# Kernel optimization log

Hardware: AMD Instinct MI355X
Metric: run time of the kernel (lower is better)

Reference implementation:

```python
import jax, jax.numpy as jnp
import numpy as np

B, T, E = 4, 2048, 1024
H, D = 16, 64


def setup_inputs() -> dict:
    key = jax.random.key(0)
    ks = jax.random.split(key, 7)
    scale = 1.0 / np.sqrt(E)
    return {
        "query": jax.random.normal(ks[0], (B, T, E), jnp.float32),
        "key_": jax.random.normal(ks[1], (B, T, E), jnp.float32),
        "value": jax.random.normal(ks[2], (B, T, E), jnp.float32),
        # nn.Linear weights have shape (out_features, in_features); y = x @ W.T
        "Wq": jax.random.normal(ks[3], (H * D, E), jnp.float32) * scale,
        "Wk": jax.random.normal(ks[4], (H * D, E), jnp.float32) * scale,
        "Wv": jax.random.normal(ks[5], (H * D, E), jnp.float32) * scale,
        "Wo": jax.random.normal(ks[6], (E, H * D), jnp.float32) * scale,
    }


def reference(query, key_, value, Wq, Wk, Wv, Wo):
    # eval mode: dropout is identity
    Bq, Tq, _ = query.shape
    Q = (query @ Wq.T).reshape(Bq, Tq, H, D).transpose(0, 2, 1, 3)   # [B,H,T,D]
    K = (key_ @ Wk.T).reshape(Bq, -1, H, D).transpose(0, 2, 1, 3)    # [B,H,S,D]
    V = (value @ Wv.T).reshape(Bq, -1, H, D).transpose(0, 2, 1, 3)   # [B,H,S,D]
    scores = jnp.einsum("bhtd,bhsd->bhts", Q, K) / jnp.sqrt(jnp.float32(D))
    attn_prob = jax.nn.softmax(scores, axis=-1)                      # [B,H,T,S]
    attn_vec = jnp.einsum("bhts,bhsd->bhtd", attn_prob, V)           # [B,H,T,D]
    x = attn_vec.transpose(0, 2, 1, 3).reshape(Bq, Tq, H * D) @ Wo.T # [B,T,E]
    # need_weights=True, average_attn_weights=True -> mean over heads
    return x, attn_prob.mean(axis=1)
```

## Files before the change

kernel.cpp:

```cpp
#include <hip/hip_runtime.h>
#include <math.h>

#define HH 16
#define DD 64
#define TS 2048
#define EE 1024
#define BB 4
#define MS 12.0f

typedef __attribute__((ext_vector_type(8))) __bf16 bf16x8;
typedef __attribute__((ext_vector_type(2))) __bf16 bf16x2;
typedef __attribute__((ext_vector_type(8))) _Float16 f16x8;
typedef __attribute__((ext_vector_type(4))) float f32x4;

#if defined(__has_builtin)
#if __has_builtin(__builtin_amdgcn_fdot2_f32_bf16)
#define HAS_DOT2 1
#endif
#if __has_builtin(__builtin_amdgcn_exp2f)
#define EXP2(x) __builtin_amdgcn_exp2f(x)
#endif
#endif
#ifndef EXP2
#define EXP2(x) exp2f(x)
#endif

__device__ __forceinline__ float pexp(float c) {
    return EXP2(__builtin_fmaf(c, 0.18033688011112042f, -17.312340490667562f));
}

#define LBAR() asm volatile("s_waitcnt lgkmcnt(0)\n\ts_barrier" ::: "memory")

__device__ __forceinline__ f32x4 mm3(bf16x8 ah, bf16x8 al, bf16x8 bh, bf16x8 bl, f32x4 c) {
    c = __builtin_amdgcn_mfma_f32_16x16x32_bf16(ah, bh, c, 0, 0, 0);
    c = __builtin_amdgcn_mfma_f32_16x16x32_bf16(ah, bl, c, 0, 0, 0);
    c = __builtin_amdgcn_mfma_f32_16x16x32_bf16(al, bh, c, 0, 0, 0);
    return c;
}

__device__ __forceinline__ void gll16(const void* g, void* l) {
    __builtin_amdgcn_global_load_lds(
        (const __attribute__((address_space(1))) unsigned int*)g,
        (__attribute__((address_space(3))) unsigned int*)l, 16, 0, 0);
}

__device__ __forceinline__ unsigned pk2(float p) {
    unsigned pu = __builtin_bit_cast(unsigned, p);
    unsigned hb = pu & 0xffff0000u;
    float l = p - __builtin_bit_cast(float, hb);
    __bf16 lb = (__bf16)l;
    return hb | (unsigned)__builtin_bit_cast(unsigned short, lb);
}
__device__ __forceinline__ float upk_hi(unsigned u) { return __builtin_bit_cast(float, u & 0xffff0000u); }
__device__ __forceinline__ float upk_lo(unsigned u) { return __builtin_bit_cast(float, u << 16); }

__device__ __forceinline__ bf16x8 sel_frag(uint4 a, uint4 b, unsigned s) {
    uint4 r;
    r.x = __builtin_amdgcn_perm(a.y, a.x, s);
    r.y = __builtin_amdgcn_perm(a.w, a.z, s);
    r.z = __builtin_amdgcn_perm(b.y, b.x, s);
    r.w = __builtin_amdgcn_perm(b.w, b.z, s);
    return __builtin_bit_cast(bf16x8, r);
}

__device__ __forceinline__ void split8(const float* __restrict__ src,
    __bf16* __restrict__ hi, __bf16* __restrict__ lo, size_t i)
{
    float4 a = *(const float4*)(src + i);
    float4 b = *(const float4*)(src + i + 4);
    float v[8] = {a.x, a.y, a.z, a.w, b.x, b.y, b.z, b.w};
    bf16x8 h, l;
    #pragma unroll
    for (int j = 0; j < 8; ++j) {
        __bf16 x = (__bf16)v[j];
        h[j] = x;
        l[j] = (__bf16)(v[j] - (float)x);
    }
    *(bf16x8*)(hi + i) = h;
    *(bf16x8*)(lo + i) = l;
}

__global__ __launch_bounds__(256) void splitAll(
    const float* __restrict__ q, const float* __restrict__ k, const float* __restrict__ v,
    const float* __restrict__ wq, const float* __restrict__ wk,
    const float* __restrict__ wv, const float* __restrict__ wo,
    __bf16* __restrict__ xqh, __bf16* __restrict__ xql,
    __bf16* __restrict__ xkh, __bf16* __restrict__ xkl,
    __bf16* __restrict__ xvh, __bf16* __restrict__ xvl,
    __bf16* __restrict__ wqh, __bf16* __restrict__ wql,
    __bf16* __restrict__ wkh, __bf16* __restrict__ wkl,
    __bf16* __restrict__ wvh, __bf16* __restrict__ wvl,
    __bf16* __restrict__ woh, __bf16* __restrict__ wol)
{
    const int id = blockIdx.x;
    const float* src;
    __bf16 *hi, *lo;
    size_t base;
    if (id < 12288) {
        int z = id >> 12, loc = id & 4095;
        src = z == 0 ? q : z == 1 ? k : v;
        hi  = z == 0 ? xqh : z == 1 ? xkh : xvh;
        lo  = z == 0 ? xql : z == 1 ? xkl : xvl;
        base = (size_t)loc * 2048;
    } else {
        int w = (id - 12288) >> 9, loc = (id - 12288) & 511;
        src = w == 0 ? wq : w == 1 ? wk : w == 2 ? wv : wo;
        hi  = w == 0 ? wqh : w == 1 ? wkh : w == 2 ? wvh : woh;
        lo  = w == 0 ? wql : w == 1 ? wkl : w == 2 ? wvl : wol;
        base = (size_t)loc * 2048;
    }
    split8(src, hi, lo, base + threadIdx.x * 8);
}

__global__ __launch_bounds__(256) void gemmQKV(
    const __bf16* __restrict__ xqh, const __bf16* __restrict__ xql,
    const __bf16* __restrict__ xkh, const __bf16* __restrict__ xkl,
    const __bf16* __restrict__ xvh, const __bf16* __restrict__ xvl,
    const __bf16* __restrict__ wqh, const __bf16* __restrict__ wql,
    const __bf16* __restrict__ wkh, const __bf16* __restrict__ wkl,
    const __bf16* __restrict__ wvh, const __bf16* __restrict__ wvl,
    __bf16* __restrict__ Qh, __bf16* __restrict__ Ql,
    __bf16* __restrict__ Kh, __bf16* __restrict__ Kl,
    __bf16* __restrict__ Vh, __bf16* __restrict__ Vl)
{
    const int z = blockIdx.z;
    const __bf16* Ah = z == 0 ? xqh : z == 1 ? xkh : xvh;
    const __bf16* Al = z == 0 ? xql : z == 1 ? xkl : xvl;
    const __bf16* Bh = z == 0 ? wqh : z == 1 ? wkh : wvh;
    const __bf16* Bl = z == 0 ? wql : z == 1 ? wkl : wvl;
    __bf16* Ch = z == 0 ? Qh : z == 1 ? Kh : Vh;
    __bf16* Cl = z == 0 ? Ql : z == 1 ? Kl : Vl;
    const int K = EE;

    __shared__ __bf16 sA[2][128 * 32];
    __shared__ __bf16 sB[2][128 * 32];
    const int tid = threadIdx.x, wave = tid >> 6, lane = tid & 63;
    const int quad = lane >> 4, l15 = lane & 15;
    const int m0 = blockIdx.y * 128, n0 = blockIdx.x * 128;
    const int wm = (wave >> 1) * 64, wn = (wave & 1) * 64;
    const int srow = lane >> 2, scol = (lane & 3) * 8;

    f32x4 acc[4][4];
    #pragma unroll
    for (int i = 0; i < 4; ++i)
        #pragma unroll
        for (int j = 0; j < 4; ++j)
            acc[i][j] = (f32x4){0.f, 0.f, 0.f, 0.f};

    for (int k0 = 0; k0 < K; k0 += 32) {
        __syncthreads();
        #pragma unroll
        for (int i = 0; i < 2; ++i) {
            int c = wave * 2 + i;
            size_t ga = (size_t)(m0 + c * 16 + srow) * K + k0 + scol;
            size_t gb = (size_t)(n0 + c * 16 + srow) * K + k0 + scol;
            gll16(Ah + ga, &sA[0][c * 512]);
            gll16(Al + ga, &sA[1][c * 512]);
            gll16(Bh + gb, &sB[0][c * 512]);
            gll16(Bl + gb, &sB[1][c * 512]);
        }
        __syncthreads();
        bf16x8 fAh[4], fAl[4], fBh[4], fBl[4];
        #pragma unroll
        for (int mb = 0; mb < 4; ++mb) {
            int r = (wm + mb * 16 + l15) * 32 + quad * 8;
            fAh[mb] = *(const bf16x8*)&sA[0][r];
            fAl[mb] = *(const bf16x8*)&sA[1][r];
        }
        #pragma unroll
        for (int nb = 0; nb < 4; ++nb) {
            int r = (wn + nb * 16 + l15) * 32 + quad * 8;
            fBh[nb] = *(const bf16x8*)&sB[0][r];
            fBl[nb] = *(const bf16x8*)&sB[1][r];
        }
        #pragma unroll
        for (int mb = 0; mb < 4; ++mb)
            #pragma unroll
            for (int nb = 0; nb < 4; ++nb)
                acc[mb][nb] = mm3(fAh[mb], fAl[mb], fBh[nb], fBl[nb], acc[mb][nb]);
    }

    #pragma unroll
    for (int mb = 0; mb < 4; ++mb)
        #pragma unroll
        for (int nb = 0; nb < 4; ++nb)
            #pragma unroll
            for (int r = 0; r < 4; ++r) {
                int m = m0 + wm + mb * 16 + quad * 4 + r;
                int n = n0 + wn + nb * 16 + l15;
                float v = acc[mb][nb][r];
                int b = m >> 11, t = m & (TS - 1);
                int h = n >> 6,  d = n & (DD - 1);
                __bf16 hi = (__bf16)v;
                __bf16 lo = (__bf16)(v - (float)hi);
                size_t hbase = ((size_t)b * HH + h) * TS * DD;
                size_t off;
                if (z == 2)
                    off = hbase + (size_t)(((d >> 4) * 64 + (t >> 5)) * 512
                          + (((t >> 3) & 3) * 16 + (d & 15)) * 8 + (t & 7));
                else
                    off = hbase + (size_t)(((t >> 4) * 2 + (d >> 5)) * 512
                          + (((d >> 3) & 3) * 16 + (t & 15)) * 8 + (d & 7));
                Ch[off] = hi;
                Cl[off] = lo;
            }
}

__global__ __launch_bounds__(256) void attnF(
    const __bf16* __restrict__ Qh, const __bf16* __restrict__ Ql,
    const __bf16* __restrict__ Kh, const __bf16* __restrict__ Kl,
    const __bf16* __restrict__ VhT, const __bf16* __restrict__ VlT,
    __bf16* __restrict__ avh, __bf16* __restrict__ avl,
    float* __restrict__ out1, _Float16* __restrict__ pp)
{
    __shared__ unsigned Pt[4][32][68];
    const int tid = threadIdx.x, wave = tid >> 6, lane = tid & 63;
    const int quad = lane >> 4, l15 = lane & 15;
    const int linear = blockIdx.x + 64 * blockIdx.y + 256 * blockIdx.z;
    const int bg = (linear & 7) + 8 * (linear >> 9);
    const int tt = (linear >> 3) & 63;
    const int b = bg & 3, g = bg >> 2;
    const int t0 = tt * 32;
    const int h = g * 4 + wave;
    const size_t hoff = (size_t)(b * HH + h);
    const __bf16* qhp = Qh + hoff * TS * DD;
    const __bf16* qlp = Ql + hoff * TS * DD;
    const __bf16* khp = Kh + hoff * TS * DD;
    const __bf16* klp = Kl + hoff * TS * DD;
    const __bf16* vhp = VhT + hoff * DD * TS;
    const __bf16* vlp = VlT + hoff * DD * TS;
    _Float16* myp = pp + (size_t)(g - 1) * ((size_t)BB * TS * TS);

    const int loff = (quad * 16 + l15) * 8;

    bf16x8 fqh[2][2], fql[2][2];
    #pragma unroll
    for (int tb = 0; tb < 2; ++tb)
        #pragma unroll
        for (int ks = 0; ks < 2; ++ks) {
            size_t o = (size_t)((((t0 >> 4) + tb) * 2 + ks) * 512 + loff);
            fqh[tb][ks] = *(const bf16x8*)(qhp + o);
            fql[tb][ks] = *(const bf16x8*)(qlp + o);
        }

    float lacc[2][4];
    #pragma unroll
    for (int tb = 0; tb < 2; ++tb)
        #pragma unroll
        for (int r = 0; r < 4; ++r) lacc[tb][r] = 0.f;

    for (int st = 0; st < 32; ++st) {
        bf16x8 kh[4][2], kl[4][2];
        #pragma unroll
        for (int sb = 0; sb < 4; ++sb) {
            const int kt = ((st * 4 + sb) * 2) * 512 + loff;
            kh[sb][0] = *(const bf16x8*)(khp + kt);
            kh[sb][1] = *(const bf16x8*)(khp + kt + 512);
            kl[sb][0] = *(const bf16x8*)(klp + kt);
            kl[sb][1] = *(const bf16x8*)(klp + kt + 512);
        }
        #pragma unroll
        for (int sb = 0; sb < 4; ++sb)
            #pragma unroll
            for (int tb = 0; tb < 2; ++tb) {
                f32x4 c = (f32x4){0.f, 0.f, 0.f, 0.f};
                __builtin_amdgcn_s_setprio(1);
                c = mm3(fqh[tb][0], fql[tb][0], kh[sb][0], kl[sb][0], c);
                c = mm3(fqh[tb][1], fql[tb][1], kh[sb][1], kl[sb][1], c);
                __builtin_amdgcn_s_setprio(0);
                #pragma unroll
                for (int r = 0; r < 4; ++r)
                    lacc[tb][r] += pexp(c[r]);
            }
    }
    float rf[2][4];
    #pragma unroll
    for (int tb = 0; tb < 2; ++tb)
        #pragma unroll
        for (int r = 0; r < 4; ++r) {
            float v = lacc[tb][r];
            v += __shfl_xor(v, 1);
            v += __shfl_xor(v, 2);
            v += __shfl_xor(v, 4);
            v += __shfl_xor(v, 8);
            rf[tb][r] = 1.0f / v;
        }

    f32x4 oacc[2][4];
    #pragma unroll
    for (int tb = 0; tb < 2; ++tb)
        #pragma unroll
        for (int db = 0; db < 4; ++db) oacc[tb][db] = (f32x4){0.f, 0.f, 0.f, 0.f};

    for (int st = 0; st < 32; ++st) {
        bf16x8 kh[4][2], kl[4][2];
        #pragma unroll
        for (int sb = 0; sb < 4; ++sb) {
            const int kt = ((st * 4 + sb) * 2) * 512 + loff;
            kh[sb][0] = *(const bf16x8*)(khp + kt);
            kh[sb][1] = *(const bf16x8*)(khp + kt + 512);
            kl[sb][0] = *(const bf16x8*)(klp + kt);
            kl[sb][1] = *(const bf16x8*)(klp + kt + 512);
        }
        #pragma unroll
        for (int sb = 0; sb < 4; ++sb)
            #pragma unroll
            for (int tb = 0; tb < 2; ++tb) {
                f32x4 c = (f32x4){0.f, 0.f, 0.f, 0.f};
                __builtin_amdgcn_s_setprio(1);
                c = mm3(fqh[tb][0], fql[tb][0], kh[sb][0], kl[sb][0], c);
                c = mm3(fqh[tb][1], fql[tb][1], kh[sb][1], kl[sb][1], c);
                __builtin_amdgcn_s_setprio(0);
                #pragma unroll
                for (int r = 0; r < 4; ++r) {
                    float p = pexp(c[r]) * rf[tb][r];
                    Pt[wave][tb * 16 + quad * 4 + r][sb * 16 + l15] = pk2(p);
                }
            }
        LBAR();

        bf16x8 vh[4][2], vl[4][2];
        #pragma unroll
        for (int db = 0; db < 4; ++db) {
            const int vt = (db * 64 + st * 2) * 512 + loff;
            vh[db][0] = *(const bf16x8*)(vhp + vt);
            vh[db][1] = *(const bf16x8*)(vhp + vt + 512);
            vl[db][0] = *(const bf16x8*)(vlp + vt);
            vl[db][1] = *(const bf16x8*)(vlp + vt + 512);
        }

        bf16x8 fph[2][2], fpl[2][2];
        #pragma unroll
        for (int tb = 0; tb < 2; ++tb)
            #pragma unroll
            for (int ks = 0; ks < 2; ++ks) {
                const unsigned* ppt = &Pt[wave][tb * 16 + l15][ks * 32 + quad * 8];
                uint4 a = *(const uint4*)ppt;
                uint4 bq = *(const uint4*)(ppt + 4);
                fph[tb][ks] = sel_frag(a, bq, 0x07060302u);
                fpl[tb][ks] = sel_frag(a, bq, 0x05040100u);
            }

        {
            int row = tid >> 3, s8 = (tid & 7) * 8;
            float vs[8] = {0.f, 0.f, 0.f, 0.f, 0.f, 0.f, 0.f, 0.f};
#ifdef HAS_DOT2
            const bf16x2 w2 = {(__bf16)0.0625f, (__bf16)0.0625f};
#endif
            #pragma unroll
            for (int w = 0; w < 4; ++w) {
                const unsigned* pw = &Pt[w][row][s8];
                uint4 a = *(const uint4*)pw;
                uint4 bq = *(const uint4*)(pw + 4);
                unsigned uu[8] = {a.x, a.y, a.z, a.w, bq.x, bq.y, bq.z, bq.w};
                #pragma unroll
                for (int j = 0; j < 8; ++j) {
#ifdef HAS_DOT2
                    vs[j] = __builtin_amdgcn_fdot2_f32_bf16(
                        __builtin_bit_cast(bf16x2, uu[j]), w2, vs[j], false);
#else
                    vs[j] += (upk_hi(uu[j]) + upk_lo(uu[j])) * 0.0625f;
#endif
                }
            }
            size_t off = ((size_t)b * TS + t0 + row) * TS + st * 64 + s8;
            if (g == 0) {
                float4 o0, o1v;
                o0.x = vs[0]; o0.y = vs[1]; o0.z = vs[2]; o0.w = vs[3];
                o1v.x = vs[4]; o1v.y = vs[5]; o1v.z = vs[6]; o1v.w = vs[7];
                *(float4*)(out1 + off) = o0;
                *(float4*)(out1 + off + 4) = o1v;
            } else {
                f16x8 hv;
                #pragma unroll
                for (int j = 0; j < 8; ++j)
                    hv[j] = (_Float16)vs[j];
                *(f16x8*)(myp + off) = hv;
            }
        }

        __builtin_amdgcn_s_setprio(1);
        #pragma unroll
        for (int db = 0; db < 4; ++db)
            #pragma unroll
            for (int tb = 0; tb < 2; ++tb) {
                f32x4 o = oacc[tb][db];
                o = mm3(fph[tb][0], fpl[tb][0], vh[db][0], vl[db][0], o);
                o = mm3(fph[tb][1], fpl[tb][1], vh[db][1], vl[db][1], o);
                oacc[tb][db] = o;
            }
        __builtin_amdgcn_s_setprio(0);
        LBAR();
    }

    #pragma unroll
    for (int tb = 0; tb < 2; ++tb)
        #pragma unroll
        for (int db = 0; db < 4; ++db)
            #pragma unroll
            for (int r = 0; r < 4; ++r) {
                int row = t0 + tb * 16 + quad * 4 + r;
                int col = h * 64 + db * 16 + l15;
                float v = oacc[tb][db][r];
                __bf16 hi = (__bf16)v;
                size_t o = ((size_t)b * TS + row) * EE + col;
                avh[o] = hi;
                avl[o] = (__bf16)(v - (float)hi);
            }
}

__global__ __launch_bounds__(256) void gemmO(
    const __bf16* __restrict__ Ah, const __bf16* __restrict__ Al,
    const __bf16* __restrict__ Bh, const __bf16* __restrict__ Bl,
    float* __restrict__ Cf, float* __restrict__ out1,
    const _Float16* __restrict__ pp, int M, int N, int K)
{
    __shared__ __bf16 sA[2][128 * 32];
    __shared__ __bf16 sB[2][128 * 32];
    const int tid = threadIdx.x;

    if (blockIdx.x >= 8) {
        const size_t P = (size_t)BB * TS * TS;
        size_t r = (size_t)(blockIdx.x - 8) + 128 * blockIdx.y;
        size_t i = (r * 256 + tid) * 8;
        float4 a = *(const float4*)(out1 + i);
        float4 c = *(const float4*)(out1 + i + 4);
        f16x8 q1 = *(const f16x8*)(pp + i);
        f16x8 q2 = *(const f16x8*)(pp + P + i);
        f16x8 q3 = *(const f16x8*)(pp + 2 * P + i);
        a.x += (float)q1[0] + (float)q2[0] + (float)q3[0];
        a.y += (float)q1[1] + (float)q2[1] + (float)q3[1];
        a.z += (float)q1[2] + (float)q2[2] + (float)q3[2];
        a.w += (float)q1[3] + (float)q2[3] + (float)q3[3];
        c.x += (float)q1[4] + (float)q2[4] + (float)q3[4];
        c.y += (float)q1[5] + (float)q2[5] + (float)q3[5];
        c.z += (float)q1[6] + (float)q2[6] + (float)q3[6];
        c.w += (float)q1[7] + (float)q2[7] + (float)q3[7];
        *(float4*)(out1 + i) = a;
        *(float4*)(out1 + i + 4) = c;
        return;
    }

    const int wave = tid >> 6, lane = tid & 63;
    const int quad = lane >> 4, l15 = lane & 15;
    const int m0 = blockIdx.y * 128, n0 = blockIdx.x * 128;
    const int wm = (wave >> 1) * 64, wn = (wave & 1) * 64;
    const int srow = lane >> 2, scol = (lane & 3) * 8;

    f32x4 acc[4][4];
    #pragma unroll
    for (int i = 0; i < 4; ++i)
        #pragma unroll
        for (int j = 0; j < 4; ++j)
            acc[i][j] = (f32x4){0.f, 0.f, 0.f, 0.f};

    for (int k0 = 0; k0 < K; k0 += 32) {
        __syncthreads();
        #pragma unroll
        for (int i = 0; i < 2; ++i) {
            int c = wave * 2 + i;
            size_t ga = (size_t)(m0 + c * 16 + srow) * K + k0 + scol;
            size_t gb = (size_t)(n0 + c * 16 + srow) * K + k0 + scol;
            gll16(Ah + ga, &sA[0][c * 512]);
            gll16(Al + ga, &sA[1][c * 512]);
            gll16(Bh + gb, &sB[0][c * 512]);
            gll16(Bl + gb, &sB[1][c * 512]);
        }
        __syncthreads();
        bf16x8 fAh[4], fAl[4], fBh[4], fBl[4];
        #pragma unroll
        for (int mb = 0; mb < 4; ++mb) {
            int r = (wm + mb * 16 + l15) * 32 + quad * 8;
            fAh[mb] = *(const bf16x8*)&sA[0][r];
            fAl[mb] = *(const bf16x8*)&sA[1][r];
        }
        #pragma unroll
        for (int nb = 0; nb < 4; ++nb) {
            int r = (wn + nb * 16 + l15) * 32 + quad * 8;
            fBh[nb] = *(const bf16x8*)&sB[0][r];
            fBl[nb] = *(const bf16x8*)&sB[1][r];
        }
        #pragma unroll
        for (int mb = 0; mb < 4; ++mb)
            #pragma unroll
            for (int nb = 0; nb < 4; ++nb)
                acc[mb][nb] = mm3(fAh[mb], fAl[mb], fBh[nb], fBl[nb], acc[mb][nb]);
    }

    #pragma unroll
    for (int mb = 0; mb < 4; ++mb)
        #pragma unroll
        for (int nb = 0; nb < 4; ++nb)
            #pragma unroll
            for (int r = 0; r < 4; ++r) {
                int m = m0 + wm + mb * 16 + quad * 4 + r;
                int n = n0 + wn + nb * 16 + l15;
                Cf[(size_t)m * N + n] = acc[mb][nb][r];
            }
}

extern "C" void kernel_launch(void* const* d_in, const int* in_sizes, int n_in,
                              void* d_out, int out_size, void* d_ws, size_t ws_size,
                              hipStream_t stream)
{
    const float* query = (const float*)d_in[0];
    const float* key_  = (const float*)d_in[1];
    const float* value = (const float*)d_in[2];
    const float* Wq    = (const float*)d_in[3];
    const float* Wk    = (const float*)d_in[4];
    const float* Wv    = (const float*)d_in[5];
    const float* Wo    = (const float*)d_in[6];

    float* out0 = (float*)d_out;
    float* out1 = out0 + (size_t)BB * TS * EE;

    char* base = (char*)d_ws;
    const size_t U = 16777216;
    __bf16* xqh = (__bf16*)(base + 0 * U);
    __bf16* xql = (__bf16*)(base + 1 * U);
    __bf16* xkh = (__bf16*)(base + 2 * U);
    __bf16* xkl = (__bf16*)(base + 3 * U);
    __bf16* xvh = (__bf16*)(base + 4 * U);
    __bf16* xvl = (__bf16*)(base + 5 * U);
    __bf16* Qhp = (__bf16*)(base + 6 * U);
    __bf16* Qlp = (__bf16*)(base + 7 * U);
    __bf16* Khp = (__bf16*)(base + 8 * U);
    __bf16* Klp = (__bf16*)(base + 9 * U);
    __bf16* VhT = (__bf16*)(base + 10 * U);
    __bf16* VlT = (__bf16*)(base + 11 * U);
    __bf16* avh = (__bf16*)(base + 12 * U);
    __bf16* avl = (__bf16*)(base + 13 * U);
    __bf16* wqh = (__bf16*)(base + 14 * U);
    __bf16* wql = wqh + 1048576;
    __bf16* wkh = wql + 1048576;
    __bf16* wkl = wkh + 1048576;
    __bf16* wvh = wkl + 1048576;
    __bf16* wvl = wvh + 1048576;
    __bf16* woh = wvl + 1048576;
    __bf16* wol = woh + 1048576;
    _Float16* pp = (_Float16*)(base + 0 * U);

    splitAll<<<14336, 256, 0, stream>>>(query, key_, value, Wq, Wk, Wv, Wo,
                                        xqh, xql, xkh, xkl, xvh, xvl,
                                        wqh, wql, wkh, wkl, wvh, wvl, woh, wol);

    gemmQKV<<<dim3(8, 64, 3), 256, 0, stream>>>(xqh, xql, xkh, xkl, xvh, xvl,
                                                wqh, wql, wkh, wkl, wvh, wvl,
                                                Qhp, Qlp, Khp, Klp, VhT, VlT);

    attnF<<<dim3(64, 4, 4), 256, 0, stream>>>(Qhp, Qlp, Khp, Klp, VhT, VlT,
                                              avh, avl, out1, pp);

    gemmO<<<dim3(136, 64), 256, 0, stream>>>(avh, avl, woh, wol, out0, out1, pp,
                                             8192, 1024, 1024);
}
```

Baseline: 857.3 us.

## Overlap V projection GEMM with softmax denominator pass in one fused launch

Splits the attention kernel's first pass (row-sum of exp scores, i.e. softmax denominators) into a separate kernel that shares a launch with the V projection GEMM. Blocks are interleaved 8 GEMM tiles to 16 denominator tiles per group of 24. The denominators are written to a global buffer and read back by the second-pass attention kernel. The QKV GEMM now computes only Q and K. This is meant to fill the GPU with independent work and overlap compute-bound GEMM with the exp-heavy pass, at the cost of an extra global buffer round-trip and one more kernel launch.

```diff
diff --git a/kernel.cpp b/kernel.cpp
--- a/kernel.cpp
+++ b/kernel.cpp
@@ -206,10 +206,169 @@
             }
 }
 
-__global__ __launch_bounds__(256) void attnF(
+__global__ __launch_bounds__(256) void gvpa(
+    const __bf16* __restrict__ xvh, const __bf16* __restrict__ xvl,
+    const __bf16* __restrict__ wvh, const __bf16* __restrict__ wvl,
+    __bf16* __restrict__ Vh, __bf16* __restrict__ Vl,
+    const __bf16* __restrict__ Qh, const __bf16* __restrict__ Ql,
+    const __bf16* __restrict__ Kh, const __bf16* __restrict__ Kl,
+    float* __restrict__ rfg)
+{
+    __shared__ __bf16 sA[2][128 * 32];
+    __shared__ __bf16 sB[2][128 * 32];
+    const int tid = threadIdx.x, wave = tid >> 6, lane = tid & 63;
+    const int quad = lane >> 4, l15 = lane & 15;
+    const int bid = blockIdx.x;
+    const int group = bid / 24, rem = bid % 24;
+
+    if (rem >= 8) {
+        const int x = bid & 7;
+        const int rk = group * 2 + ((rem - 8) >> 3);
+        const int bg = x + 8 * (rk >> 6);
+        const int tt = rk & 63;
+        const int b = bg & 3, g = bg >> 2;
+        const int t0 = tt * 32;
+        const int h = g * 4 + wave;
+        const size_t hoff = (size_t)(b * HH + h);
+        const __bf16* qhp = Qh + hoff * TS * DD;
+        const __bf16* qlp = Ql + hoff * TS * DD;
+        const __bf16* khp = Kh + hoff * TS * DD;
+        const __bf16* klp = Kl + hoff * TS * DD;
+        const int loff = (quad * 16 + l15) * 8;
+
+        bf16x8 fqh[2][2], fql[2][2];
+        #pragma unroll
+        for (int tb = 0; tb < 2; ++tb)
+            #pragma unroll
+            for (int ks = 0; ks < 2; ++ks) {
+                size_t o = (size_t)((((t0 >> 4) + tb) * 2 + ks) * 512 + loff);
+                fqh[tb][ks] = *(const bf16x8*)(qhp + o);
+                fql[tb][ks] = *(const bf16x8*)(qlp + o);
+            }
+
+        float lacc[2][4];
+        #pragma unroll
+        for (int tb = 0; tb < 2; ++tb)
+            #pragma unroll
+            for (int r = 0; r < 4; ++r) lacc[tb][r] = 0.f;
+
+        for (int st = 0; st < 32; ++st) {
+            bf16x8 kh[4][2], kl[4][2];
+            #pragma unroll
+            for (int sb = 0; sb < 4; ++sb) {
+                const int kt = ((st * 4 + sb) * 2) * 512 + loff;
+                kh[sb][0] = *(const bf16x8*)(khp + kt);
+                kh[sb][1] = *(const bf16x8*)(khp + kt + 512);
+                kl[sb][0] = *(const bf16x8*)(klp + kt);
+                kl[sb][1] = *(const bf16x8*)(klp + kt + 512);
+            }
+            #pragma unroll
+            for (int sb = 0; sb < 4; ++sb)
+                #pragma unroll
+                for (int tb = 0; tb < 2; ++tb) {
+                    f32x4 c = (f32x4){0.f, 0.f, 0.f, 0.f};
+                    __builtin_amdgcn_s_setprio(1);
+                    c = mm3(fqh[tb][0], fql[tb][0], kh[sb][0], kl[sb][0], c);
+                    c = mm3(fqh[tb][1], fql[tb][1], kh[sb][1], kl[sb][1], c);
+                    __builtin_amdgcn_s_setprio(0);
+                    #pragma unroll
+                    for (int r = 0; r < 4; ++r)
+                        lacc[tb][r] += pexp(c[r]);
+                }
+        }
+        #pragma unroll
+        for (int tb = 0; tb < 2; ++tb) {
+            float rf4[4];
+            #pragma unroll
+            for (int r = 0; r < 4; ++r) {
+                float v = lacc[tb][r];
+                v += __shfl_xor(v, 1);
+                v += __shfl_xor(v, 2);
+                v += __shfl_xor(v, 4);
+                v += __shfl_xor(v, 8);
+                rf4[r] = 1.0f / v;
+            }
+            if (l15 == 0) {
+                float4 o;
+                o.x = rf4[0]; o.y = rf4[1]; o.z = rf4[2]; o.w = rf4[3];
+                *(float4*)(rfg + hoff * TS + t0 + tb * 16 + quad * 4) = o;
+            }
+        }
+        return;
+    }
+
+    const int gid = group * 8 + rem;
+    const int m0 = (gid >> 3) * 128, n0 = (gid & 7) * 128;
+    const int wm = (wave >> 1) * 64, wn = (wave & 1) * 64;
+    const int srow = lane >> 2, scol = (lane & 3) * 8;
+    const int K = EE;
+
+    f32x4 acc[4][4];
+    #pragma unroll
+    for (int i = 0; i < 4; ++i)
+        #pragma unroll
+        for (int j = 0; j < 4; ++j)
+            acc[i][j] = (f32x4){0.f, 0.f, 0.f, 0.f};
+
+    for (int k0 = 0; k0 < K; k0 += 32) {
+        __syncthreads();
+        #pragma unroll
+        for (int i = 0; i < 2; ++i) {
+            int c = wave * 2 + i;
+            size_t ga = (size_t)(m0 + c * 16 + srow) * K + k0 + scol;
+            size_t gb = (size_t)(n0 + c * 16 + srow) * K + k0 + scol;
+            gll16(xvh + ga, &sA[0][c * 512]);
+            gll16(xvl + ga, &sA[1][c * 512]);
+            gll16(wvh + gb, &sB[0][c * 512]);
+            gll16(wvl + gb, &sB[1][c * 512]);
+        }
+        __syncthreads();
+        bf16x8 fAh[4], fAl[4], fBh[4], fBl[4];
+        #pragma unroll
+        for (int mb = 0; mb < 4; ++mb) {
+            int r = (wm + mb * 16 + l15) * 32 + quad * 8;
+            fAh[mb] = *(const bf16x8*)&sA[0][r];
+            fAl[mb] = *(const bf16x8*)&sA[1][r];
+        }
+        #pragma unroll
+        for (int nb = 0; nb < 4; ++nb) {
+            int r = (wn + nb * 16 + l15) * 32 + quad * 8;
+            fBh[nb] = *(const bf16x8*)&sB[0][r];
+            fBl[nb] = *(const bf16x8*)&sB[1][r];
+        }
+        #pragma unroll
+        for (int mb = 0; mb < 4; ++mb)
+            #pragma unroll
+            for (int nb = 0; nb < 4; ++nb)
+                acc[mb][nb] = mm3(fAh[mb], fAl[mb], fBh[nb], fBl[nb], acc[mb][nb]);
+    }
+
+    #pragma unroll
+    for (int mb = 0; mb < 4; ++mb)
+        #pragma unroll
+        for (int nb = 0; nb < 4; ++nb)
+            #pragma unroll
+            for (int r = 0; r < 4; ++r) {
+                int m = m0 + wm + mb * 16 + quad * 4 + r;
+                int n = n0 + wn + nb * 16 + l15;
+                float v = acc[mb][nb][r];
+                int b = m >> 11, t = m & (TS - 1);
+                int h = n >> 6,  d = n & (DD - 1);
+                __bf16 hi = (__bf16)v;
+                __bf16 lo = (__bf16)(v - (float)hi);
+                size_t hbase = ((size_t)b * HH + h) * TS * DD;
+                size_t off = hbase + (size_t)(((d >> 4) * 64 + (t >> 5)) * 512
+                             + (((t >> 3) & 3) * 16 + (d & 15)) * 8 + (t & 7));
+                Vh[off] = hi;
+                Vl[off] = lo;
+            }
+}
+
+__global__ __launch_bounds__(256) void attnB(
     const __bf16* __restrict__ Qh, const __bf16* __restrict__ Ql,
     const __bf16* __restrict__ Kh, const __bf16* __restrict__ Kl,
     const __bf16* __restrict__ VhT, const __bf16* __restrict__ VlT,
+    const float* __restrict__ rfg,
     __bf16* __restrict__ avh, __bf16* __restrict__ avl,
     float* __restrict__ out1, _Float16* __restrict__ pp)
 {
@@ -243,48 +402,12 @@
             fql[tb][ks] = *(const bf16x8*)(qlp + o);
         }
 
-    float lacc[2][4];
-    #pragma unroll
-    for (int tb = 0; tb < 2; ++tb)
-        #pragma unroll
-        for (int r = 0; r < 4; ++r) lacc[tb][r] = 0.f;
-
-    for (int st = 0; st < 32; ++st) {
-        bf16x8 kh[4][2], kl[4][2];
-        #pragma unroll
-        for (int sb = 0; sb < 4; ++sb) {
-            const int kt = ((st * 4 + sb) * 2) * 512 + loff;
-            kh[sb][0] = *(const bf16x8*)(khp + kt);
-            kh[sb][1] = *(const bf16x8*)(khp + kt + 512);
-            kl[sb][0] = *(const bf16x8*)(klp + kt);
-            kl[sb][1] = *(const bf16x8*)(klp + kt + 512);
-        }
-        #pragma unroll
-        for (int sb = 0; sb < 4; ++sb)
-            #pragma unroll
-            for (int tb = 0; tb < 2; ++tb) {
-                f32x4 c = (f32x4){0.f, 0.f, 0.f, 0.f};
-                __builtin_amdgcn_s_setprio(1);
-                c = mm3(fqh[tb][0], fql[tb][0], kh[sb][0], kl[sb][0], c);
-                c = mm3(fqh[tb][1], fql[tb][1], kh[sb][1], kl[sb][1], c);
-                __builtin_amdgcn_s_setprio(0);
-                #pragma unroll
-                for (int r = 0; r < 4; ++r)
-                    lacc[tb][r] += pexp(c[r]);
-            }
-    }
     float rf[2][4];
     #pragma unroll
-    for (int tb = 0; tb < 2; ++tb)
-        #pragma unroll
-        for (int r = 0; r < 4; ++r) {
-            float v = lacc[tb][r];
-            v += __shfl_xor(v, 1);
-            v += __shfl_xor(v, 2);
-            v += __shfl_xor(v, 4);
-            v += __shfl_xor(v, 8);
-            rf[tb][r] = 1.0f / v;
-        }
+    for (int tb = 0; tb < 2; ++tb) {
+        float4 t4 = *(const float4*)(rfg + hoff * TS + t0 + tb * 16 + quad * 4);
+        rf[tb][0] = t4.x; rf[tb][1] = t4.y; rf[tb][2] = t4.z; rf[tb][3] = t4.w;
+    }
 
     f32x4 oacc[2][4];
     #pragma unroll
@@ -538,17 +661,21 @@
     __bf16* wvl = wvh + 1048576;
     __bf16* woh = wvl + 1048576;
     __bf16* wol = woh + 1048576;
+    float*  rfg = (float*)(base + 15 * U);
     _Float16* pp = (_Float16*)(base + 0 * U);
 
     splitAll<<<14336, 256, 0, stream>>>(query, key_, value, Wq, Wk, Wv, Wo,
                                         xqh, xql, xkh, xkl, xvh, xvl,
                                         wqh, wql, wkh, wkl, wvh, wvl, woh, wol);
 
-    gemmQKV<<<dim3(8, 64, 3), 256, 0, stream>>>(xqh, xql, xkh, xkl, xvh, xvl,
+    gemmQKV<<<dim3(8, 64, 2), 256, 0, stream>>>(xqh, xql, xkh, xkl, xvh, xvl,
                                                 wqh, wql, wkh, wkl, wvh, wvl,
                                                 Qhp, Qlp, Khp, Klp, VhT, VlT);
 
-    attnF<<<dim3(64, 4, 4), 256, 0, stream>>>(Qhp, Qlp, Khp, Klp, VhT, VlT,
+    gvpa<<<1536, 256, 0, stream>>>(xvh, xvl, wvh, wvl, VhT, VlT,
+                                   Qhp, Qlp, Khp, Klp, rfg);
+
+    attnB<<<dim3(64, 4, 4), 256, 0, stream>>>(Qhp, Qlp, Khp, Klp, VhT, VlT, rfg,
                                               avh, avl, out1, pp);
 
     gemmO<<<dim3(136, 64), 256, 0, stream>>>(avh, avl, woh, wol, out0, out1, pp,
```

Measured after the change: 849.9 us. About the same (-0.9%).
